# Kernel optimization log

Hardware: AMD Instinct MI355X
Metric: run time of the kernel (lower is better)

Reference implementation:

```python
import jax, jax.numpy as jnp
import numpy as np

NUM_TOKENS = 2048  # = token_limit(0.5) * seq_len(4096)


def setup_inputs() -> dict:
    key = jax.random.key(0)
    k0, k1, k2, k3 = jax.random.split(key, 4)
    B, S, D, F = 4, 4096, 2048, 8192
    return {
        "x": jax.random.normal(k0, (B, S, D), dtype=jnp.float32),
        "Wp": jax.random.normal(k1, (D, 1), dtype=jnp.float32) * (1.0 / np.sqrt(D)),
        "bp": jnp.zeros((1,), dtype=jnp.float32),
        "W1": jax.random.normal(k2, (D, F), dtype=jnp.float32) * (1.0 / np.sqrt(D)),
        "b1": jnp.zeros((F,), dtype=jnp.float32),
        "W2": jax.random.normal(k3, (F, D), dtype=jnp.float32) * (1.0 / np.sqrt(F)),
        "b2": jnp.zeros((D,), dtype=jnp.float32),
    }


def reference(x, Wp, bp, W1, b1, W2, b2):
    # Router: per-token scalar score via Linear(dim, 1)
    weights = x @ Wp + bp                      # [B, S, 1]
    # Faithful to source: softmax over dim=-1 (size-1 axis -> all ones)
    weights = jax.nn.softmax(weights, axis=-1)  # [B, S, 1]
    scores = weights[..., 0]                   # [B, S]
    # top-k token selection along the sequence axis
    _, idx = jax.lax.top_k(scores, NUM_TOKENS)  # [B, k] int32
    # gather the selected full tokens (intended semantics of the expand+gather)
    topk_tokens = jnp.take_along_axis(x, idx[:, :, None], axis=1)  # [B, k, D]
    # downstream block: transformer FFN
    h = jax.nn.gelu(topk_tokens @ W1 + b1)     # [B, k, 4D]
    out = h @ W2 + b2                          # [B, k, D]
    return out
```

## Files before the change

### kernel.cpp

```cpp
#include <hip/hip_runtime.h>
#include <hip/hip_bf16.h>

typedef unsigned int u32;
typedef unsigned short u16;

using bf16x8 = __attribute__((ext_vector_type(8))) short;
using f32x4  = __attribute__((ext_vector_type(4))) float;

#define DEVI static __device__ __forceinline__

DEVI u16 f2bf(float f) {
  __hip_bfloat16 h = __float2bfloat16(f);
  union { __hip_bfloat16 h; u16 u; } v; v.h = h;
  return v.u;
}

__global__ void k_convert_x(const float* __restrict__ x, u16* __restrict__ xb) {
  int idx = blockIdx.x * blockDim.x + threadIdx.x;
  size_t e = (size_t)idx * 4;
  int row = (int)(e >> 11);
  int d   = (int)(e & 2047);
  int b = row >> 11, t = row & 2047;
  const float4 v = *reinterpret_cast<const float4*>(
      x + ((size_t)(b * 4096 + t) * 2048 + d));
  ushort4 o;
  o.x = f2bf(v.x); o.y = f2bf(v.y); o.z = f2bf(v.z); o.w = f2bf(v.w);
  *reinterpret_cast<ushort4*>(xb + (size_t)row * 2048 + d) = o;
}

__global__ void k_transpose_bf16(const float* __restrict__ in,
                                 u16* __restrict__ out, int R, int C) {
  __shared__ u16 lds[64][66];
  const int t = threadIdx.x;
  const int tile_r = blockIdx.y * 64;
  const int tile_c = blockIdx.x * 64;
  const int cc = (t & 15) * 4;
  const int r0 = t >> 4;
#pragma unroll
  for (int i = 0; i < 4; ++i) {
    int r = r0 + i * 16;
    const float4 v = *reinterpret_cast<const float4*>(
        in + (size_t)(tile_r + r) * C + tile_c + cc);
    lds[r][cc]     = f2bf(v.x);
    lds[r][cc + 1] = f2bf(v.y);
    lds[r][cc + 2] = f2bf(v.z);
    lds[r][cc + 3] = f2bf(v.w);
  }
  __syncthreads();
  const int rr = (t & 15) * 4;
  const int c0 = t >> 4;
#pragma unroll
  for (int i = 0; i < 4; ++i) {
    int c = c0 + i * 16;
    ushort4 o;
    o.x = lds[rr][c]; o.y = lds[rr + 1][c];
    o.z = lds[rr + 2][c]; o.w = lds[rr + 3][c];
    *reinterpret_cast<ushort4*>(out + (size_t)(tile_c + c) * R + tile_r + rr) = o;
  }
}

#define GLDS16(g, l)                                                          \
  __builtin_amdgcn_global_load_lds(                                           \
      (const __attribute__((address_space(1))) u32*)(g),                      \
      (__attribute__((address_space(3))) u32*)(l), 16, 0, 0)

template <int DO_GELU, int BNPART>
DEVI void gemm_body(u16* lds, const u16* __restrict__ A,
                    const u16* __restrict__ B, const float* __restrict__ bias,
                    void* __restrict__ Cout, int M, int N, int K, int nbn,
                    int sft) {
  const int bid = blockIdx.x;
  int bm, bn;
  if (BNPART) {
    const int local = bid >> 3;
    bn = ((bid & 7) << sft) + (local & ((1 << sft) - 1));
    bm = local >> sft;
  } else {
    const int wg = (bid & 7) * (gridDim.x >> 3) + (bid >> 3);
    bm = wg / nbn; bn = wg % nbn;
  }

  const int tid  = threadIdx.x;
  const int w    = tid >> 6, lane = tid & 63;
  const int wr   = w >> 2, wcol = w & 3;
  const int l15  = lane & 15, lhi = lane >> 4;

  const size_t arow0 = (size_t)bm * 256;
  const size_t brow0 = (size_t)bn * 256;

  const int srow  = tid >> 3;
  const int scolb = ((tid & 7) * 16) ^ ((srow & 7) << 4);
  const u16* pA = A + (arow0 + srow) * (size_t)K + (scolb >> 1);
  const u16* pB = B + (brow0 + srow) * (size_t)K + (scolb >> 1);
  const int wA = w * 512;

  const u32 arow_b = (u32)((wr * 128 + l15) * 128);
  const u32 brow_b = (u32)((wcol * 64 + l15) * 128);
  const u32 axor   = (u32)((lhi * 16) ^ ((l15 & 7) << 4));
  const char* ldsb = (const char*)lds;

  f32x4 acc[8][4] = {};
  const int nk = K >> 6;

#define STAGE_PAIR(KT, PB, C)                                                 \
  do {                                                                        \
    GLDS16(pA + (size_t)(KT) * 64 + (size_t)(C) * 64 * (size_t)K,             \
           lds + (PB) * 16384 + (C) * 4096 + wA);                             \
    GLDS16(pB + (size_t)(KT) * 64 + (size_t)(C) * 64 * (size_t)K,             \
           lds + 32768 + (PB) * 16384 + (C) * 4096 + wA);                     \
  } while (0)

#define READ_A(DST, MH, ABASE)                                                \
  _Pragma("unroll") for (int m2 = 0; m2 < 4; ++m2)                            \
  _Pragma("unroll") for (int kk = 0; kk < 2; ++kk)                            \
    DST[m2][kk] = *(const bf16x8*)(ldsb + (ABASE) + arow_b +                  \
                                   ((MH)*4 + m2) * 2048 + (axor ^ (kk << 6)));

#define READ_B(DST, NH, BBASE)                                                \
  _Pragma("unroll") for (int n2 = 0; n2 < 2; ++n2)                            \
  _Pragma("unroll") for (int kk = 0; kk < 2; ++kk)                            \
    DST[n2][kk] = *(const bf16x8*)(ldsb + (BBASE) + brow_b +                  \
                                   ((NH)*2 + n2) * 2048 + (axor ^ (kk << 6)));

#define MFMA_Q(MH, NH, AREG, BREG)                                            \
  _Pragma("unroll") for (int m2 = 0; m2 < 4; ++m2)                            \
  _Pragma("unroll") for (int n2 = 0; n2 < 2; ++n2)                            \
  _Pragma("unroll") for (int kk = 0; kk < 2; ++kk)                            \
    acc[(MH)*4 + m2][(NH)*2 + n2] = __builtin_amdgcn_mfma_f32_16x16x32_bf16(  \
        AREG[m2][kk], BREG[n2][kk], acc[(MH)*4 + m2][(NH)*2 + n2], 0, 0, 0);

  STAGE_PAIR(0, 0, 0); STAGE_PAIR(0, 0, 1);
  STAGE_PAIR(0, 0, 2); STAGE_PAIR(0, 0, 3);
  if (nk > 1) {
    STAGE_PAIR(1, 1, 0); STAGE_PAIR(1, 1, 1);
    asm volatile("s_waitcnt vmcnt(4)" ::: "memory");
  } else {
    asm volatile("s_waitcnt vmcnt(0)" ::: "memory");
  }
  __builtin_amdgcn_s_barrier();

  for (int kt = 0; kt < nk; ++kt) {
    const int p = kt & 1;
    const u32 abase = (u32)p * 32768u;
    const u32 bbase = 65536u + (u32)p * 32768u;
    bf16x8 a0[4][2], a1[4][2], b0[2][2], b1[2][2];

    READ_A(a0, 0, abase);
    READ_B(b0, 0, bbase);
    READ_B(b1, 1, bbase);
    READ_A(a1, 1, abase);
    if (kt + 1 < nk) { STAGE_PAIR(kt + 1, p ^ 1, 2); STAGE_PAIR(kt + 1, p ^ 1, 3); }
    __builtin_amdgcn_sched_barrier(0);

    __builtin_amdgcn_s_setprio(1);
    MFMA_Q(0, 0, a0, b0);
    MFMA_Q(0, 1, a0, b1);
    __builtin_amdgcn_s_setprio(0);

    asm volatile("s_waitcnt lgkmcnt(0)" ::: "memory");
    __builtin_amdgcn_s_barrier();
    __builtin_amdgcn_sched_barrier(0);
    if (kt + 2 < nk) { STAGE_PAIR(kt + 2, p, 0); STAGE_PAIR(kt + 2, p, 1); }

    __builtin_amdgcn_s_setprio(1);
    MFMA_Q(1, 1, a1, b1);
    MFMA_Q(1, 0, a1, b0);
    __builtin_amdgcn_s_setprio(0);

    if (kt + 2 < nk) {
      asm volatile("s_waitcnt vmcnt(4)" ::: "memory");
    } else {
      asm volatile("s_waitcnt vmcnt(0)" ::: "memory");
    }
    __builtin_amdgcn_s_barrier();
  }

  const int colb = (int)brow0 + wcol * 64;
  float bb[4];
#pragma unroll
  for (int n = 0; n < 4; ++n) bb[n] = bias[colb + n * 16 + l15];
  const int tr = lane >> 2, tc = (lane & 3) * 16;

  if (DO_GELU) {
    u16* slot = lds + (size_t)w * 1152;
#pragma unroll
    for (int m = 0; m < 8; ++m) {
      const int rowb = (int)arow0 + wr * 128 + m * 16;
#pragma unroll
      for (int n = 0; n < 4; ++n)
#pragma unroll
        for (int r = 0; r < 4; ++r) {
          float v = acc[m][n][r] + bb[n];
          float u2 = v * (1.5957691216f + 0.0713548162f * v * v);
          float g  = v / (1.f + __expf(-u2));
          slot[(lhi * 4 + r) * 72 + n * 16 + l15] = f2bf(g);
        }
      asm volatile("s_waitcnt lgkmcnt(0)" ::: "memory");
      uint4 d0 = *(const uint4*)(slot + tr * 72 + tc);
      uint4 d1 = *(const uint4*)(slot + tr * 72 + tc + 8);
      u16* gp = (u16*)Cout + (size_t)(rowb + tr) * N + colb + tc;
      *(uint4*)gp = d0;
      *(uint4*)(gp + 8) = d1;
      asm volatile("s_waitcnt lgkmcnt(0)" ::: "memory");
    }
  } else {
    float* slotf = (float*)(void*)lds + (size_t)w * 1088;
#pragma unroll
    for (int m = 0; m < 8; ++m) {
      const int rowb = (int)arow0 + wr * 128 + m * 16;
#pragma unroll
      for (int n = 0; n < 4; ++n)
#pragma unroll
        for (int r = 0; r < 4; ++r)
          slotf[(lhi * 4 + r) * 68 + n * 16 + l15] = acc[m][n][r] + bb[n];
      asm volatile("s_waitcnt lgkmcnt(0)" ::: "memory");
      float4 f0 = *(const float4*)(slotf + tr * 68 + tc);
      float4 f1 = *(const float4*)(slotf + tr * 68 + tc + 4);
      float4 f2 = *(const float4*)(slotf + tr * 68 + tc + 8);
      float4 f3 = *(const float4*)(slotf + tr * 68 + tc + 12);
      float* gp = (float*)Cout + (size_t)(rowb + tr) * N + colb + tc;
      *(float4*)gp = f0;
      *(float4*)(gp + 4) = f1;
      *(float4*)(gp + 8) = f2;
      *(float4*)(gp + 12) = f3;
      asm volatile("s_waitcnt lgkmcnt(0)" ::: "memory");
    }
  }
#undef STAGE_PAIR
#undef READ_A
#undef READ_B
#undef MFMA_Q
}

__global__ __launch_bounds__(512, 2) void k_ffn1(
    const u16* __restrict__ A, const u16* __restrict__ B,
    const float* __restrict__ bias, void* __restrict__ Cout,
    int M, int N, int K, int nbn, int sft) {
  __shared__ __align__(64) u16 lds[65536];
  gemm_body<1, 1>(lds, A, B, bias, Cout, M, N, K, nbn, sft);
}

__global__ __launch_bounds__(512, 2) void k_ffn2(
    const u16* __restrict__ A, const u16* __restrict__ B,
    const float* __restrict__ bias, void* __restrict__ Cout,
    int M, int N, int K, int nbn, int sft) {
  __shared__ __align__(64) u16 lds[65536];
  gemm_body<0, 0>(lds, A, B, bias, Cout, M, N, K, nbn, sft);
}

extern "C" void kernel_launch(void* const* d_in, const int* in_sizes, int n_in,
                              void* d_out, int out_size, void* d_ws,
                              size_t ws_size, hipStream_t stream) {
  const float* x  = (const float*)d_in[0];
  const float* W1 = (const float*)d_in[3];
  const float* b1 = (const float*)d_in[4];
  const float* W2 = (const float*)d_in[5];
  const float* b2 = (const float*)d_in[6];
  float* out = (float*)d_out;

  char* ws = (char*)d_ws;
  u16* Xb  = (u16*)(ws);
  u16* W1T = (u16*)(ws + 33554432);
  u16* W2T = (u16*)(ws + 67108864);
  u16* H   = (u16*)(ws + 100663296);

  k_convert_x<<<16384, 256, 0, stream>>>(x, Xb);
  k_transpose_bf16<<<dim3(8192 / 64, 2048 / 64), 256, 0, stream>>>(W1, W1T, 2048, 8192);
  k_transpose_bf16<<<dim3(2048 / 64, 8192 / 64), 256, 0, stream>>>(W2, W2T, 8192, 2048);
  k_ffn1<<<1024, 512, 0, stream>>>(Xb, W1T, b1, (void*)H, 8192, 8192, 2048, 32, 2);
  k_ffn2<<<256, 512, 0, stream>>>(H, W2T, b2, (void*)out, 8192, 2048, 8192, 8, 0);
}
```

Measured before the change: 530.8 us.

## Make FFN1 persistent over four M tiles with cross-tile prefetch

The first FFN GEMM now launches 256 workgroups instead of 1024. Each workgroup keeps one B (W1T) column tile and loops over four A row tiles. The K-loop prefetch runs across tile boundaries so the next tile's first stages load while the current tile finishes, and a separate LDS region holds the GELU epilogue so it does not clash with the prefetched buffers. This targets per-workgroup prologue and epilogue bubbles and improves B-tile reuse, but LDS use grows (about 146KB), which may limit occupancy to one block per CU.

```diff
diff --git a/kernel.cpp b/kernel.cpp
--- a/kernel.cpp
+++ b/kernel.cpp
@@ -64,51 +64,13 @@
       (const __attribute__((address_space(1))) u32*)(g),                      \
       (__attribute__((address_space(3))) u32*)(l), 16, 0, 0)
 
-template <int DO_GELU, int BNPART>
-DEVI void gemm_body(u16* lds, const u16* __restrict__ A,
-                    const u16* __restrict__ B, const float* __restrict__ bias,
-                    void* __restrict__ Cout, int M, int N, int K, int nbn,
-                    int sft) {
-  const int bid = blockIdx.x;
-  int bm, bn;
-  if (BNPART) {
-    const int local = bid >> 3;
-    bn = ((bid & 7) << sft) + (local & ((1 << sft) - 1));
-    bm = local >> sft;
-  } else {
-    const int wg = (bid & 7) * (gridDim.x >> 3) + (bid >> 3);
-    bm = wg / nbn; bn = wg % nbn;
-  }
-
-  const int tid  = threadIdx.x;
-  const int w    = tid >> 6, lane = tid & 63;
-  const int wr   = w >> 2, wcol = w & 3;
-  const int l15  = lane & 15, lhi = lane >> 4;
-
-  const size_t arow0 = (size_t)bm * 256;
-  const size_t brow0 = (size_t)bn * 256;
-
-  const int srow  = tid >> 3;
-  const int scolb = ((tid & 7) * 16) ^ ((srow & 7) << 4);
-  const u16* pA = A + (arow0 + srow) * (size_t)K + (scolb >> 1);
-  const u16* pB = B + (brow0 + srow) * (size_t)K + (scolb >> 1);
-  const int wA = w * 512;
-
-  const u32 arow_b = (u32)((wr * 128 + l15) * 128);
-  const u32 brow_b = (u32)((wcol * 64 + l15) * 128);
-  const u32 axor   = (u32)((lhi * 16) ^ ((l15 & 7) << 4));
-  const char* ldsb = (const char*)lds;
-
-  f32x4 acc[8][4] = {};
-  const int nk = K >> 6;
-
-#define STAGE_PAIR(KT, PB, C)                                                 \
-  do {                                                                        \
-    GLDS16(pA + (size_t)(KT) * 64 + (size_t)(C) * 64 * (size_t)K,             \
-           lds + (PB) * 16384 + (C) * 4096 + wA);                             \
-    GLDS16(pB + (size_t)(KT) * 64 + (size_t)(C) * 64 * (size_t)K,             \
-           lds + 32768 + (PB) * 16384 + (C) * 4096 + wA);                     \
-  } while (0)
+DEVI void stage_pair(u16* lds, const u16* pA, const u16* pB, int lda, int ldb,
+                     int kt, int pb, int c, int wA) {
+  GLDS16(pA + (size_t)kt * 64 + (size_t)c * 64 * (size_t)lda,
+         lds + pb * 16384 + c * 4096 + wA);
+  GLDS16(pB + (size_t)kt * 64 + (size_t)c * 64 * (size_t)ldb,
+         lds + 32768 + pb * 16384 + c * 4096 + wA);
+}
 
 #define READ_A(DST, MH, ABASE)                                                \
   _Pragma("unroll") for (int m2 = 0; m2 < 4; ++m2)                            \
@@ -129,15 +91,181 @@
     acc[(MH)*4 + m2][(NH)*2 + n2] = __builtin_amdgcn_mfma_f32_16x16x32_bf16(  \
         AREG[m2][kk], BREG[n2][kk], acc[(MH)*4 + m2][(NH)*2 + n2], 0, 0, 0);
 
-  STAGE_PAIR(0, 0, 0); STAGE_PAIR(0, 0, 1);
-  STAGE_PAIR(0, 0, 2); STAGE_PAIR(0, 0, 3);
-  if (nk > 1) {
-    STAGE_PAIR(1, 1, 0); STAGE_PAIR(1, 1, 1);
+__global__ __launch_bounds__(512, 2) void k_ffn1(
+    const u16* __restrict__ A, const u16* __restrict__ B,
+    const float* __restrict__ bias, u16* __restrict__ Cout,
+    int N, int K) {
+  __shared__ __align__(64) u16 lds[74752];
+
+  const int bid = blockIdx.x;
+  const int xcd = bid & 7, cu = bid >> 3;
+  const int bn    = (xcd << 2) + (cu & 3);
+  const int bmrow = cu >> 2;
+
+  const int tid  = threadIdx.x;
+  const int w    = tid >> 6, lane = tid & 63;
+  const int wr   = w >> 2, wcol = w & 3;
+  const int l15  = lane & 15, lhi = lane >> 4;
+
+  const size_t brow0 = (size_t)bn * 256;
+  const int srow  = tid >> 3;
+  const int scolb = ((tid & 7) * 16) ^ ((srow & 7) << 4);
+  const size_t aoff = (size_t)srow * K + (scolb >> 1);
+  const u16* pB = B + (brow0 + srow) * (size_t)K + (scolb >> 1);
+  const int wA = w * 512;
+
+  const u32 arow_b = (u32)((wr * 128 + l15) * 128);
+  const u32 brow_b = (u32)((wcol * 64 + l15) * 128);
+  const u32 axor   = (u32)((lhi * 16) ^ ((l15 & 7) << 4));
+  const char* ldsb = (const char*)lds;
+  const int nk = K >> 6;
+
+  u16* slot = lds + 65536 + (size_t)w * 1152;
+  const int tr = lane >> 2, tc = (lane & 3) * 16;
+
+  {
+    const u16* pA0 = A + (size_t)bmrow * 256 * K + aoff;
+    stage_pair(lds, pA0, pB, K, K, 0, 0, 0, wA);
+    stage_pair(lds, pA0, pB, K, K, 0, 0, 1, wA);
+    stage_pair(lds, pA0, pB, K, K, 0, 0, 2, wA);
+    stage_pair(lds, pA0, pB, K, K, 0, 0, 3, wA);
+    stage_pair(lds, pA0, pB, K, K, 1, 1, 0, wA);
+    stage_pair(lds, pA0, pB, K, K, 1, 1, 1, wA);
     asm volatile("s_waitcnt vmcnt(4)" ::: "memory");
-  } else {
-    asm volatile("s_waitcnt vmcnt(0)" ::: "memory");
-  }
+    __builtin_amdgcn_s_barrier();
+  }
+
+  for (int g = 0; g < 4; ++g) {
+    const u16* pAc = A + (size_t)(bmrow + 8 * g) * 256 * K + aoff;
+    const u16* pAn = A + (size_t)(bmrow + 8 * (g + 1)) * 256 * K + aoff;
+    const bool hasNext = (g < 3);
+
+    f32x4 acc[8][4] = {};
+
+    for (int kt = 0; kt < nk; ++kt) {
+      const int p = kt & 1;
+      const u32 abase = (u32)p * 32768u;
+      const u32 bbase = 65536u + (u32)p * 32768u;
+      bf16x8 a0[4][2], a1[4][2], b0[2][2], b1[2][2];
+
+      READ_A(a0, 0, abase);
+      READ_B(b0, 0, bbase);
+      READ_B(b1, 1, bbase);
+      READ_A(a1, 1, abase);
+      {
+        const int t1 = kt + 1;
+        if (t1 < nk) {
+          stage_pair(lds, pAc, pB, K, K, t1, p ^ 1, 2, wA);
+          stage_pair(lds, pAc, pB, K, K, t1, p ^ 1, 3, wA);
+        } else if (hasNext) {
+          stage_pair(lds, pAn, pB, K, K, t1 - nk, p ^ 1, 2, wA);
+          stage_pair(lds, pAn, pB, K, K, t1 - nk, p ^ 1, 3, wA);
+        }
+      }
+      __builtin_amdgcn_sched_barrier(0);
+
+      __builtin_amdgcn_s_setprio(1);
+      MFMA_Q(0, 0, a0, b0);
+      MFMA_Q(0, 1, a0, b1);
+      __builtin_amdgcn_s_setprio(0);
+
+      asm volatile("s_waitcnt lgkmcnt(0)" ::: "memory");
+      __builtin_amdgcn_s_barrier();
+      __builtin_amdgcn_sched_barrier(0);
+      bool staged2 = false;
+      {
+        const int t2 = kt + 2;
+        if (t2 < nk) {
+          stage_pair(lds, pAc, pB, K, K, t2, p, 0, wA);
+          stage_pair(lds, pAc, pB, K, K, t2, p, 1, wA);
+          staged2 = true;
+        } else if (hasNext) {
+          stage_pair(lds, pAn, pB, K, K, t2 - nk, p, 0, wA);
+          stage_pair(lds, pAn, pB, K, K, t2 - nk, p, 1, wA);
+          staged2 = true;
+        }
+      }
+
+      __builtin_amdgcn_s_setprio(1);
+      MFMA_Q(1, 1, a1, b1);
+      MFMA_Q(1, 0, a1, b0);
+      __builtin_amdgcn_s_setprio(0);
+
+      if (staged2) {
+        asm volatile("s_waitcnt vmcnt(4)" ::: "memory");
+      } else {
+        asm volatile("s_waitcnt vmcnt(0)" ::: "memory");
+      }
+      __builtin_amdgcn_s_barrier();
+    }
+
+    const int arow0 = (bmrow + 8 * g) * 256;
+    const int colb  = (int)brow0 + wcol * 64;
+    float bb[4];
+#pragma unroll
+    for (int n = 0; n < 4; ++n) bb[n] = bias[colb + n * 16 + l15];
+#pragma unroll
+    for (int m = 0; m < 8; ++m) {
+      const int rowb = arow0 + wr * 128 + m * 16;
+#pragma unroll
+      for (int n = 0; n < 4; ++n)
+#pragma unroll
+        for (int r = 0; r < 4; ++r) {
+          float v = acc[m][n][r] + bb[n];
+          float u2 = v * (1.5957691216f + 0.0713548162f * v * v);
+          float gl = v / (1.f + __expf(-u2));
+          slot[(lhi * 4 + r) * 72 + n * 16 + l15] = f2bf(gl);
+        }
+      asm volatile("s_waitcnt lgkmcnt(0)" ::: "memory");
+      uint4 d0 = *(const uint4*)(slot + tr * 72 + tc);
+      uint4 d1 = *(const uint4*)(slot + tr * 72 + tc + 8);
+      u16* gp = Cout + (size_t)(rowb + tr) * N + colb + tc;
+      *(uint4*)gp = d0;
+      *(uint4*)(gp + 8) = d1;
+      asm volatile("s_waitcnt lgkmcnt(0)" ::: "memory");
+    }
+  }
+}
+
+__global__ __launch_bounds__(512, 2) void k_ffn2(
+    const u16* __restrict__ A, const u16* __restrict__ B,
+    const float* __restrict__ bias, float* __restrict__ Cout,
+    int N, int K, int nbn) {
+  __shared__ __align__(64) u16 lds[65536];
+
+  const int bid = blockIdx.x;
+  const int wg  = (bid & 7) * (gridDim.x >> 3) + (bid >> 3);
+  const int bm = wg / nbn, bn = wg % nbn;
+
+  const int tid  = threadIdx.x;
+  const int w    = tid >> 6, lane = tid & 63;
+  const int wr   = w >> 2, wcol = w & 3;
+  const int l15  = lane & 15, lhi = lane >> 4;
+
+  const size_t arow0 = (size_t)bm * 256;
+  const size_t brow0 = (size_t)bn * 256;
+  const int srow  = tid >> 3;
+  const int scolb = ((tid & 7) * 16) ^ ((srow & 7) << 4);
+  const u16* pA = A + (arow0 + srow) * (size_t)K + (scolb >> 1);
+  const u16* pB = B + (brow0 + srow) * (size_t)K + (scolb >> 1);
+  const int wA = w * 512;
+
+  const u32 arow_b = (u32)((wr * 128 + l15) * 128);
+  const u32 brow_b = (u32)((wcol * 64 + l15) * 128);
+  const u32 axor   = (u32)((lhi * 16) ^ ((l15 & 7) << 4));
+  const char* ldsb = (const char*)lds;
+  const int nk = K >> 6;
+
+  stage_pair(lds, pA, pB, K, K, 0, 0, 0, wA);
+  stage_pair(lds, pA, pB, K, K, 0, 0, 1, wA);
+  stage_pair(lds, pA, pB, K, K, 0, 0, 2, wA);
+  stage_pair(lds, pA, pB, K, K, 0, 0, 3, wA);
+  stage_pair(lds, pA, pB, K, K, 1, 1, 0, wA);
+  stage_pair(lds, pA, pB, K, K, 1, 1, 1, wA);
+  asm volatile("s_waitcnt vmcnt(4)" ::: "memory");
   __builtin_amdgcn_s_barrier();
+
+  f32x4 acc[8][4] = {};
 
   for (int kt = 0; kt < nk; ++kt) {
     const int p = kt & 1;
@@ -149,7 +277,10 @@
     READ_B(b0, 0, bbase);
     READ_B(b1, 1, bbase);
     READ_A(a1, 1, abase);
-    if (kt + 1 < nk) { STAGE_PAIR(kt + 1, p ^ 1, 2); STAGE_PAIR(kt + 1, p ^ 1, 3); }
+    if (kt + 1 < nk) {
+      stage_pair(lds, pA, pB, K, K, kt + 1, p ^ 1, 2, wA);
+      stage_pair(lds, pA, pB, K, K, kt + 1, p ^ 1, 3, wA);
+    }
     __builtin_amdgcn_sched_barrier(0);
 
     __builtin_amdgcn_s_setprio(1);
@@ -160,7 +291,10 @@
     asm volatile("s_waitcnt lgkmcnt(0)" ::: "memory");
     __builtin_amdgcn_s_barrier();
     __builtin_amdgcn_sched_barrier(0);
-    if (kt + 2 < nk) { STAGE_PAIR(kt + 2, p, 0); STAGE_PAIR(kt + 2, p, 1); }
+    if (kt + 2 < nk) {
+      stage_pair(lds, pA, pB, K, K, kt + 2, p, 0, wA);
+      stage_pair(lds, pA, pB, K, K, kt + 2, p, 1, wA);
+    }
 
     __builtin_amdgcn_s_setprio(1);
     MFMA_Q(1, 1, a1, b1);
@@ -180,72 +314,27 @@
 #pragma unroll
   for (int n = 0; n < 4; ++n) bb[n] = bias[colb + n * 16 + l15];
   const int tr = lane >> 2, tc = (lane & 3) * 16;
-
-  if (DO_GELU) {
-    u16* slot = lds + (size_t)w * 1152;
-#pragma unroll
-    for (int m = 0; m < 8; ++m) {
-      const int rowb = (int)arow0 + wr * 128 + m * 16;
-#pragma unroll
-      for (int n = 0; n < 4; ++n)
-#pragma unroll
-        for (int r = 0; r < 4; ++r) {
-          float v = acc[m][n][r] + bb[n];
-          float u2 = v * (1.5957691216f + 0.0713548162f * v * v);
-          float g  = v / (1.f + __expf(-u2));
-          slot[(lhi * 4 + r) * 72 + n * 16 + l15] = f2bf(g);
-        }
-      asm volatile("s_waitcnt lgkmcnt(0)" ::: "memory");
-      uint4 d0 = *(const uint4*)(slot + tr * 72 + tc);
-      uint4 d1 = *(const uint4*)(slot + tr * 72 + tc + 8);
-      u16* gp = (u16*)Cout + (size_t)(rowb + tr) * N + colb + tc;
-      *(uint4*)gp = d0;
-      *(uint4*)(gp + 8) = d1;
-      asm volatile("s_waitcnt lgkmcnt(0)" ::: "memory");
-    }
-  } else {
-    float* slotf = (float*)(void*)lds + (size_t)w * 1088;
-#pragma unroll
-    for (int m = 0; m < 8; ++m) {
-      const int rowb = (int)arow0 + wr * 128 + m * 16;
-#pragma unroll
-      for (int n = 0; n < 4; ++n)
-#pragma unroll
-        for (int r = 0; r < 4; ++r)
-          slotf[(lhi * 4 + r) * 68 + n * 16 + l15] = acc[m][n][r] + bb[n];
-      asm volatile("s_waitcnt lgkmcnt(0)" ::: "memory");
-      float4 f0 = *(const float4*)(slotf + tr * 68 + tc);
-      float4 f1 = *(const float4*)(slotf + tr * 68 + tc + 4);
-      float4 f2 = *(const float4*)(slotf + tr * 68 + tc + 8);
-      float4 f3 = *(const float4*)(slotf + tr * 68 + tc + 12);
-      float* gp = (float*)Cout + (size_t)(rowb + tr) * N + colb + tc;
-      *(float4*)gp = f0;
-      *(float4*)(gp + 4) = f1;
-      *(float4*)(gp + 8) = f2;
-      *(float4*)(gp + 12) = f3;
-      asm volatile("s_waitcnt lgkmcnt(0)" ::: "memory");
-    }
-  }
-#undef STAGE_PAIR
-#undef READ_A
-#undef READ_B
-#undef MFMA_Q
-}
-
-__global__ __launch_bounds__(512, 2) void k_ffn1(
-    const u16* __restrict__ A, const u16* __restrict__ B,
-    const float* __restrict__ bias, void* __restrict__ Cout,
-    int M, int N, int K, int nbn, int sft) {
-  __shared__ __align__(64) u16 lds[65536];
-  gemm_body<1, 1>(lds, A, B, bias, Cout, M, N, K, nbn, sft);
-}
-
-__global__ __launch_bounds__(512, 2) void k_ffn2(
-    const u16* __restrict__ A, const u16* __restrict__ B,
-    const float* __restrict__ bias, void* __restrict__ Cout,
-    int M, int N, int K, int nbn, int sft) {
-  __shared__ __align__(64) u16 lds[65536];
-  gemm_body<0, 0>(lds, A, B, bias, Cout, M, N, K, nbn, sft);
+  float* slotf = (float*)(void*)lds + (size_t)w * 1088;
+#pragma unroll
+  for (int m = 0; m < 8; ++m) {
+    const int rowb = (int)arow0 + wr * 128 + m * 16;
+#pragma unroll
+    for (int n = 0; n < 4; ++n)
+#pragma unroll
+      for (int r = 0; r < 4; ++r)
+        slotf[(lhi * 4 + r) * 68 + n * 16 + l15] = acc[m][n][r] + bb[n];
+    asm volatile("s_waitcnt lgkmcnt(0)" ::: "memory");
+    float4 f0 = *(const float4*)(slotf + tr * 68 + tc);
+    float4 f1 = *(const float4*)(slotf + tr * 68 + tc + 4);
+    float4 f2 = *(const float4*)(slotf + tr * 68 + tc + 8);
+    float4 f3 = *(const float4*)(slotf + tr * 68 + tc + 12);
+    float* gp = Cout + (size_t)(rowb + tr) * N + colb + tc;
+    *(float4*)gp = f0;
+    *(float4*)(gp + 4) = f1;
+    *(float4*)(gp + 8) = f2;
+    *(float4*)(gp + 12) = f3;
+    asm volatile("s_waitcnt lgkmcnt(0)" ::: "memory");
+  }
 }
 
 extern "C" void kernel_launch(void* const* d_in, const int* in_sizes, int n_in,
@@ -267,6 +356,6 @@
   k_convert_x<<<16384, 256, 0, stream>>>(x, Xb);
   k_transpose_bf16<<<dim3(8192 / 64, 2048 / 64), 256, 0, stream>>>(W1, W1T, 2048, 8192);
   k_transpose_bf16<<<dim3(2048 / 64, 8192 / 64), 256, 0, stream>>>(W2, W2T, 8192, 2048);
-  k_ffn1<<<1024, 512, 0, stream>>>(Xb, W1T, b1, (void*)H, 8192, 8192, 2048, 32, 2);
-  k_ffn2<<<256, 512, 0, stream>>>(H, W2T, b2, (void*)out, 8192, 2048, 8192, 8, 0);
-}
+  k_ffn1<<<256, 512, 0, stream>>>(Xb, W1T, b1, H, 8192, 2048);
+  k_ffn2<<<256, 512, 0, stream>>>(H, W2T, b2, out, 2048, 8192, 8);
+}
```

Result: no change. 530.3 us (median of 2 runs) (-0.1%).
